# Kernel tuning notes

Hardware: AMD Instinct MI355X
Metric: run time of the kernel (lower is better)

Reference implementation:

```python
import jax, jax.numpy as jnp
import numpy as np

N_CODES, N_EDGES, EMB, N_C, NNZ = 4096, 8192, 128, 4, 65536
ADD_RATIO, TEMP = 0.1, 0.5
MASK_VAL = -1e9


def setup_inputs() -> dict:
    key = jax.random.key(0)
    k1, k2, k3, k4, k5 = jax.random.split(key, 5)
    X = jax.random.normal(k1, (N_CODES, EMB), jnp.float32)
    V = jax.random.randint(k2, (NNZ,), 0, N_CODES)
    E = jax.random.randint(k3, (NNZ,), 0, N_EDGES)
    # incidence matrix has 1s exactly at the (V, E) nonzero entries
    H = jnp.zeros((N_CODES, N_EDGES), jnp.float32).at[V, E].set(1.0)
    p = jnp.clip(jax.random.uniform(k4, (N_CODES, N_EDGES), jnp.float32), 0.05, 0.95)
    cos_weight = jax.random.normal(k5, (N_C, EMB), jnp.float32)
    return {"X": X, "H": H, "V": V, "E": E,
            "incident_mask_prob": p, "cos_weight": cos_weight}


def _l2norm(x):
    # F.normalize(x, p=2, dim=-1, eps=1e-6): x / max(||x||, eps)
    n = jnp.sqrt(jnp.sum(x * x, axis=-1, keepdims=True))
    return x / jnp.maximum(n, 1e-6)


def reference(X, H, V, E, incident_mask_prob, cos_weight):
    num_edges = H.shape[1]
    n_c = cos_weight.shape[0]
    # 1) edge embeddings: scatter-mean of incident code embeddings
    sums = jax.ops.segment_sum(X[V], E, num_segments=num_edges)      # (M, D)
    cnt = jax.ops.segment_sum(jnp.ones((V.shape[0],), X.dtype), E,
                              num_segments=num_edges)                 # (M,)
    eX = sums / jnp.maximum(cnt, 1.0)[:, None]
    # 2) multi-head cosine similarity, mean over heads
    node_m = _l2norm(X[:, None, :] * cos_weight[None])               # (N, h, D)
    edge_m = _l2norm(eX[:, None, :] * cos_weight[None])              # (M, h, D)
    S = jnp.einsum('nhd,mhd->nm', node_m, edge_m) / n_c              # (N, M)
    # mask out existing incidences
    S = S.at[V, E].set(MASK_VAL)
    # 3) global top-k new incidences (k is static)
    k = int(ADD_RATIO * V.shape[0])
    _, idx = jax.lax.top_k(S.reshape(-1), k)
    row = idx // num_edges
    col = idx % num_edges
    delta_H = jnp.zeros_like(H).at[row, col].set(1.0)
    enriched_H = H + delta_H
    # 4) RelaxedBernoulli(temperature, probs).rsample()
    u = jax.random.uniform(jax.random.key(42), H.shape, H.dtype,
                           minval=1e-6, maxval=1.0 - 1e-6)
    logits = (jnp.log(incident_mask_prob) - jnp.log1p(-incident_mask_prob)
              + jnp.log(u) - jnp.log1p(-u)) / TEMP
    incident_mask = jax.nn.sigmoid(logits)
    return enriched_H * incident_mask
```

## Files before the change

### kernel.cpp

```cpp
#include <hip/hip_runtime.h>
#include <math.h>

#define N_CODES 4096
#define N_EDGES 8192
#define EMB     128
#define NHEAD   4
#define NNZ     65536
#define K_TOP   6553
#define S_TOTAL 33554432
#define NBINS   8192
#define CAP2    131072
#define SLACK_BINS 12
#define TIE_CAP 1024

typedef _Float16 f16_t;
typedef __attribute__((ext_vector_type(8))) _Float16 f16x8;
typedef __attribute__((ext_vector_type(4))) float f32x4;

__device__ __forceinline__ unsigned rotl32(unsigned v, int r) {
  return (v << r) | (v >> (32 - r));
}

__device__ float jax_u42(unsigned pos) {
  const unsigned ks0 = 0u, ks1 = 42u, ks2 = 0x1BD11BDAu ^ 0u ^ 42u;
  unsigned x0 = 0u  + ks0;
  unsigned x1 = pos + ks1;
#define TFR(r) { x0 += x1; x1 = rotl32(x1, (r)); x1 ^= x0; }
  TFR(13) TFR(15) TFR(26) TFR(6)   x0 += ks1; x1 += ks2 + 1u;
  TFR(17) TFR(29) TFR(16) TFR(24)  x0 += ks2; x1 += ks0 + 2u;
  TFR(13) TFR(15) TFR(26) TFR(6)   x0 += ks0; x1 += ks1 + 3u;
  TFR(17) TFR(29) TFR(16) TFR(24)  x0 += ks1; x1 += ks2 + 4u;
  TFR(13) TFR(15) TFR(26) TFR(6)   x0 += ks2; x1 += ks0 + 5u;
#undef TFR
  unsigned bits = x0 ^ x1;
  unsigned fb = (bits >> 9) | 0x3f800000u;
  float f = __uint_as_float(fb) - 1.0f;
  const float minv = 1e-6f;
  const float maxv = (float)(1.0 - 1e-6);
  float u = f * (maxv - minv) + minv;
  return fmaxf(minv, u);
}

__device__ float mask_val(float p, unsigned pos) {
  float u = jax_u42(pos);
  float l = (logf(p) - log1pf(-p) + logf(u) - log1pf(-u)) * 2.0f;
  return 1.0f / (1.0f + expf(-l));
}

__device__ __forceinline__ unsigned long long f64key(double v) {
  long long b = __double_as_longlong(v);
  return (b < 0) ? ~(unsigned long long)b
                 : ((unsigned long long)b | 0x8000000000000000ULL);
}

__global__ void count_k(const int* __restrict__ E, int* __restrict__ cnt) {
  int i = blockIdx.x * blockDim.x + threadIdx.x;
  if (i < NNZ) atomicAdd(&cnt[E[i]], 1);
}

__global__ __launch_bounds__(1024) void scan_k(const int* __restrict__ cnt,
                                               int* __restrict__ offs) {
  __shared__ int part[1024];
  int t = threadIdx.x;
  int local[8]; int s = 0;
  for (int j = 0; j < 8; ++j) { local[j] = cnt[t * 8 + j]; s += local[j]; }
  part[t] = s; __syncthreads();
  int v = s;
  for (int o = 1; o < 1024; o <<= 1) {
    int add = (t >= o) ? part[t - o] : 0;
    __syncthreads();
    v += add; part[t] = v;
    __syncthreads();
  }
  int base = v - s;
  for (int j = 0; j < 8; ++j) { offs[t * 8 + j] = base; base += local[j]; }
}

__global__ void scatter_k(const int* __restrict__ E, const int* __restrict__ offs,
                          int* __restrict__ cursor, int* __restrict__ bucket) {
  int i = blockIdx.x * blockDim.x + threadIdx.x;
  if (i < NNZ) {
    int e = E[i];
    int p = atomicAdd(&cursor[e], 1);
    bucket[offs[e] + p] = i;
  }
}

__global__ __launch_bounds__(128) void edge_k(const float* __restrict__ X,
                                              const int* __restrict__ V,
                                              const int* __restrict__ cnt,
                                              const int* __restrict__ offs,
                                              int* __restrict__ bucket,
                                              const float* __restrict__ W,
                                              f16_t* __restrict__ B16) {
  __shared__ int lst[512];
  __shared__ float red[2];
  int m = blockIdx.x, t = threadIdx.x;
  int deg = cnt[m], off = offs[m];
  int n = min(deg, 512);
  for (int j = t; j < n; j += 128) lst[j] = bucket[off + j];
  __syncthreads();
  if (t == 0 && n > 1) {
    for (int a = 1; a < n; ++a) {
      int key = lst[a]; int b = a - 1;
      while (b >= 0 && lst[b] > key) { lst[b + 1] = lst[b]; --b; }
      lst[b + 1] = key;
    }
  }
  __syncthreads();
  for (int j = t; j < n; j += 128) bucket[off + j] = lst[j];
  float s = 0.f;
  for (int j = 0; j < n; ++j) s += X[(size_t)V[lst[j]] * EMB + t];
  float eXd = s / fmaxf((float)deg, 1.0f);
  int lane = t & 63, wv = t >> 6;
  for (int h = 0; h < NHEAD; ++h) {
    float wd = W[h * EMB + t];
    float val = eXd * wd;
    float ss = val * val;
    for (int o = 32; o > 0; o >>= 1) ss += __shfl_down(ss, o, 64);
    if (lane == 0) red[wv] = ss;
    __syncthreads();
    float nh = 1.0f / fmaxf(sqrtf(red[0] + red[1]), 1e-6f);
    B16[(size_t)m * (NHEAD * EMB) + h * EMB + t] = (f16_t)(eXd * wd * wd * nh);
    __syncthreads();
  }
}

__global__ __launch_bounds__(128) void node_k(const float* __restrict__ X,
                                              const float* __restrict__ W,
                                              f16_t* __restrict__ A16) {
  __shared__ float red[2];
  int nid = blockIdx.x, t = threadIdx.x;
  float xd = X[(size_t)nid * EMB + t];
  int lane = t & 63, wv = t >> 6;
  for (int h = 0; h < NHEAD; ++h) {
    float val = xd * W[h * EMB + t];
    float ss = val * val;
    for (int o = 32; o > 0; o >>= 1) ss += __shfl_down(ss, o, 64);
    if (lane == 0) red[wv] = ss;
    __syncthreads();
    float nh = 1.0f / fmaxf(sqrtf(red[0] + red[1]), 1e-6f);
    A16[(size_t)nid * (NHEAD * EMB) + h * EMB + t] = (f16_t)(xd * nh);
    __syncthreads();
  }
}

__global__ __launch_bounds__(256) void gemm_mfma(const f16_t* __restrict__ A16,
                                                 const f16_t* __restrict__ B16,
                                                 float* __restrict__ C) {
  __shared__ __align__(16) f16_t As[128 * 32];
  __shared__ __align__(16) f16_t Bs[128 * 32];
  const int tid  = threadIdx.x;
  const int lane = tid & 63;
  const int wv   = tid >> 6;
  const int m0   = blockIdx.x * 128;
  const int n0   = blockIdx.y * 128;
  const int wr   = (wv >> 1) * 64;
  const int wc   = (wv & 1) * 64;
  const int frow = lane & 15;
  const int fg   = lane >> 4;
  const int sw   = (frow >> 1) & 3;
  const int fo   = ((fg ^ sw) << 3);

  f32x4 acc[4][4];
#pragma unroll
  for (int i = 0; i < 4; ++i)
#pragma unroll
    for (int j = 0; j < 4; ++j) acc[i][j] = (f32x4){0.f, 0.f, 0.f, 0.f};

  for (int k0 = 0; k0 < 512; k0 += 32) {
    __syncthreads();
#pragma unroll
    for (int r = 0; r < 2; ++r) {
      int chunk = r * 256 + wv * 64 + lane;
      int row   = chunk >> 2;
      int cb    = ((chunk & 3) ^ ((chunk >> 3) & 3)) << 3;
      __builtin_amdgcn_global_load_lds(
          (const __attribute__((address_space(1))) void*)
              (A16 + ((size_t)(n0 + row) << 9) + k0 + cb),
          (__attribute__((address_space(3))) void*)
              (As + (size_t)(r * 256 + wv * 64) * 8),
          16, 0, 0);
      __builtin_amdgcn_global_load_lds(
          (const __attribute__((address_space(1))) void*)
              (B16 + ((size_t)(m0 + row) << 9) + k0 + cb),
          (__attribute__((address_space(3))) void*)
              (Bs + (size_t)(r * 256 + wv * 64) * 8),
          16, 0, 0);
    }
    __syncthreads();
    f16x8 a[4], b[4];
#pragma unroll
    for (int i = 0; i < 4; ++i)
      a[i] = *(const f16x8*)(As + (wr + i * 16 + frow) * 32 + fo);
#pragma unroll
    for (int j = 0; j < 4; ++j)
      b[j] = *(const f16x8*)(Bs + (wc + j * 16 + frow) * 32 + fo);
#pragma unroll
    for (int i = 0; i < 4; ++i)
#pragma unroll
      for (int j = 0; j < 4; ++j)
        acc[i][j] = __builtin_amdgcn_mfma_f32_16x16x32_f16(a[i], b[j], acc[i][j], 0, 0, 0);
  }
#pragma unroll
  for (int i = 0; i < 4; ++i)
#pragma unroll
    for (int q = 0; q < 4; ++q) {
      int row = n0 + wr + i * 16 + fg * 4 + q;
      float* Cr = C + (size_t)row * N_EDGES + m0 + wc;
#pragma unroll
      for (int j = 0; j < 4; ++j)
        Cr[j * 16 + frow] = acc[i][j][q] * 0.25f;
    }
}

__global__ void maskset_k(const int* __restrict__ V, const int* __restrict__ E,
                          float* __restrict__ S) {
  int i = blockIdx.x * blockDim.x + threadIdx.x;
  if (i < NNZ) S[(size_t)V[i] * N_EDGES + E[i]] = -1e9f;
}

__global__ __launch_bounds__(256) void hist_k(const float4* __restrict__ S4,
                                              unsigned* __restrict__ ghist) {
  __shared__ unsigned hh[NBINS];
  for (int i = threadIdx.x; i < NBINS; i += 256) hh[i] = 0;
  __syncthreads();
  int stride = gridDim.x * blockDim.x;
  for (int i = blockIdx.x * blockDim.x + threadIdx.x; i < S_TOTAL / 4; i += stride) {
    float4 v = S4[i];
    float vv[4] = {v.x, v.y, v.z, v.w};
#pragma unroll
    for (int c = 0; c < 4; ++c) {
      float bf = fminf(fmaxf((vv[c] + 1.0f) * 4096.0f, 0.0f), (float)(NBINS - 1));
      atomicAdd(&hh[(int)bf], 1u);
    }
  }
  __syncthreads();
  for (int i = threadIdx.x; i < NBINS; i += 256)
    if (hh[i]) atomicAdd(&ghist[i], hh[i]);
}

__global__ __launch_bounds__(1024) void thresh_k(const unsigned* __restrict__ hist,
                                                 float* __restrict__ T_lo) {
  __shared__ unsigned suff[1024];
  int t = threadIdx.x;
  const int G = NBINS / 1024;
  int b0 = t * G;
  unsigned s = 0;
  for (int j = 0; j < G; ++j) s += hist[b0 + j];
  unsigned v = s;
  suff[t] = v; __syncthreads();
  for (int o = 1; o < 1024; o <<= 1) {
    unsigned add = (t + o < 1024) ? suff[t + o] : 0u;
    __syncthreads();
    v += add; suff[t] = v;
    __syncthreads();
  }
  unsigned above = (t < 1023) ? suff[t + 1] : 0u;
  if (above < (unsigned)K_TOP && suff[t] >= (unsigned)K_TOP) {
    unsigned running = above;
    int B = b0;
    for (int b = b0 + G - 1; b >= b0; --b) {
      running += hist[b];
      if (running >= (unsigned)K_TOP) { B = b; break; }
    }
    B = max(B, SLACK_BINS);
    *T_lo = (float)(B - SLACK_BINS) * (1.0f / 4096.0f) - 1.0f;
  }
}

__global__ void collect_k(const float4* __restrict__ S4, const float* __restrict__ T_lo_p,
                          unsigned* __restrict__ counter, int* __restrict__ ci) {
  float T = *T_lo_p;
  int stride = gridDim.x * blockDim.x;
  for (int i = blockIdx.x * blockDim.x + threadIdx.x; i < S_TOTAL / 4; i += stride) {
    float4 v = S4[i];
    float vv[4] = {v.x, v.y, v.z, v.w};
#pragma unroll
    for (int c = 0; c < 4; ++c) {
      if (vv[c] >= T) {
        unsigned j = atomicAdd(counter, 1u);
        if (j < CAP2) ci[j] = i * 4 + c;
      }
    }
  }
}

__global__ __launch_bounds__(256) void rescore_k(const float* __restrict__ X,
                                                 const float* __restrict__ W,
                                                 const int* __restrict__ V,
                                                 const int* __restrict__ cnt,
                                                 const int* __restrict__ offs,
                                                 const int* __restrict__ bucket,
                                                 const int* __restrict__ ci,
                                                 const unsigned* __restrict__ counter,
                                                 unsigned long long* __restrict__ ckey) {
  int C = (int)min(*counter, (unsigned)CAP2);
  int wave = threadIdx.x >> 6, lane = threadIdx.x & 63;
  int j = blockIdx.x * 4 + wave;
  if (j >= C) return;
  int pos = ci[j];
  int n = pos >> 13;
  int m = pos & 8191;
  int deg = cnt[m], off = offs[m];
  int nmem = min(deg, 512);
  double e0 = 0.0, e1 = 0.0;
  for (int q = 0; q < nmem; ++q) {
    const float* xv = X + (size_t)V[bucket[off + q]] * EMB;
    e0 += (double)xv[lane];
    e1 += (double)xv[lane + 64];
  }
  double dd = fmax((double)deg, 1.0);
  e0 /= dd; e1 /= dd;
  const float* xr = X + (size_t)n * EMB;
  double x0 = (double)xr[lane], x1 = (double)xr[lane + 64];
  double s = 0.0;
  for (int h = 0; h < NHEAD; ++h) {
    const float* wr = W + h * EMB;
    double w0 = (double)wr[lane], w1 = (double)wr[lane + 64];
    double xw0 = x0 * w0, xw1 = x1 * w1;
    double ew0 = e0 * w0, ew1 = e1 * w1;
    double an = xw0 * xw0 + xw1 * xw1;
    double ae = ew0 * ew0 + ew1 * ew1;
    double dt = xw0 * ew0 + xw1 * ew1;
    for (int o = 32; o > 0; o >>= 1) {
      an += __shfl_down(an, o, 64);
      ae += __shfl_down(ae, o, 64);
      dt += __shfl_down(dt, o, 64);
    }
    if (lane == 0) {
      double Nn = fmax(sqrt(an), 1e-6);
      double Ne = fmax(sqrt(ae), 1e-6);
      s += dt / (Nn * Ne);
    }
  }
  if (lane == 0) ckey[j] = f64key(s * 0.25);
}

__global__ __launch_bounds__(1024) void kth_k(const unsigned long long* __restrict__ keys,
                                              const unsigned* __restrict__ counter,
                                              unsigned long long* __restrict__ thr) {
  __shared__ unsigned hist[256];
  __shared__ unsigned long long s_prefix;
  __shared__ unsigned s_kleft, s_cgreat;
  int C = (int)min(*counter, (unsigned)CAP2);
  if (threadIdx.x == 0) { s_prefix = 0ULL; s_kleft = K_TOP; s_cgreat = 0u; }
  __syncthreads();
  for (int level = 7; level >= 0; --level) {
    for (int i = threadIdx.x; i < 256; i += 1024) hist[i] = 0;
    __syncthreads();
    unsigned long long prefix = s_prefix;
    unsigned long long pmask = (level == 7) ? 0ULL : (~0ULL << ((level + 1) * 8));
    for (int i = threadIdx.x; i < C; i += 1024) {
      unsigned long long k = keys[i];
      if ((k & pmask) == prefix)
        atomicAdd(&hist[(unsigned)((k >> (level * 8)) & 0xFF)], 1u);
    }
    __syncthreads();
    if (threadIdx.x == 0) {
      unsigned cum = 0; int b = 0;
      for (int i = 255; i >= 0; --i) {
        if (cum + hist[i] >= s_kleft) { b = i; break; }
        cum += hist[i];
      }
      s_prefix |= ((unsigned long long)b << (level * 8));
      s_kleft  -= cum;
      s_cgreat += cum;
    }
    __syncthreads();
  }
  if (threadIdx.x == 0) { thr[0] = s_prefix; thr[1] = (unsigned long long)s_cgreat; }
}

__global__ void write_k(const unsigned long long* __restrict__ keys,
                        const int* __restrict__ ci,
                        const unsigned* __restrict__ counter,
                        const unsigned long long* __restrict__ thr,
                        const float* __restrict__ P, float* __restrict__ out,
                        int* __restrict__ tiebuf, unsigned* __restrict__ tiecnt) {
  int C = (int)min(*counter, (unsigned)CAP2);
  int j = blockIdx.x * blockDim.x + threadIdx.x;
  if (j >= C) return;
  unsigned long long k = keys[j];
  unsigned long long t = thr[0];
  if (k > t) {
    unsigned pos = (unsigned)ci[j];
    out[pos] = mask_val(P[pos], pos);
  } else if (k == t) {
    unsigned q = atomicAdd(tiecnt, 1u);
    if (q < TIE_CAP) tiebuf[q] = ci[j];
  }
}

__global__ __launch_bounds__(256) void tiefin_k(const int* __restrict__ tiebuf,
                                                const unsigned* __restrict__ tiecnt,
                                                const unsigned long long* __restrict__ thr,
                                                const float* __restrict__ P,
                                                float* __restrict__ out) {
  __shared__ int idx[TIE_CAP];
  int T = (int)min(*tiecnt, (unsigned)TIE_CAP);
  int need = K_TOP - (int)thr[1];
  if (need <= 0 || T == 0) return;
  for (int i = threadIdx.x; i < T; i += 256) idx[i] = tiebuf[i];
  __syncthreads();
  if (threadIdx.x == 0 && T > 1) {
    for (int a = 1; a < T; ++a) {
      int key = idx[a]; int b = a - 1;
      while (b >= 0 && idx[b] > key) { idx[b + 1] = idx[b]; --b; }
      idx[b + 1] = key;
    }
  }
  __syncthreads();
  int m = min(need, T);
  for (int i = threadIdx.x; i < m; i += 256) {
    unsigned pos = (unsigned)idx[i];
    out[pos] = mask_val(P[pos], pos);
  }
}

__global__ void scatterH_k(const int* __restrict__ V, const int* __restrict__ E,
                           const float* __restrict__ P, float* __restrict__ out) {
  int i = blockIdx.x * blockDim.x + threadIdx.x;
  if (i >= NNZ) return;
  unsigned pos = (unsigned)V[i] * (unsigned)N_EDGES + (unsigned)E[i];
  out[pos] = mask_val(P[pos], pos);
}

extern "C" void kernel_launch(void* const* d_in, const int* in_sizes, int n_in,
                              void* d_out, int out_size, void* d_ws, size_t ws_size,
                              hipStream_t stream) {
  const float* X = (const float*)d_in[0];
  const int*   V = (const int*)d_in[2];
  const int*   E = (const int*)d_in[3];
  const float* P = (const float*)d_in[4];
  const float* W = (const float*)d_in[5];
  float* S = (float*)d_out;

  char* w = (char*)d_ws;
  int*      cnt      = (int*)(w + 0);
  int*      offs     = (int*)(w + 32768);
  int*      cursor   = (int*)(w + 65536);
  int*      bucket   = (int*)(w + 98304);
  unsigned* hist     = (unsigned*)(w + 360448);
  unsigned* counter  = (unsigned*)(w + 393216);
  float*    T_lo     = (float*)(w + 393220);
  unsigned* tiecnt   = (unsigned*)(w + 393224);
  unsigned long long* thr = (unsigned long long*)(w + 393232);
  int*      cand_idx = (int*)(w + 393472);
  unsigned long long* cand_key = (unsigned long long*)(w + 917760);
  int*      tiebuf   = (int*)(w + 1966336);
  f16_t*    A16      = (f16_t*)(w + 1970432);
  f16_t*    B16      = (f16_t*)(w + 6164736);

  hipMemsetAsync(cnt,     0, 32768, stream);
  hipMemsetAsync(cursor,  0, 32768, stream);
  hipMemsetAsync(hist,    0, NBINS * 4, stream);
  hipMemsetAsync(counter, 0, 48, stream);

  count_k   <<<NNZ / 256, 256, 0, stream>>>(E, cnt);
  scan_k    <<<1, 1024, 0, stream>>>(cnt, offs);
  scatter_k <<<NNZ / 256, 256, 0, stream>>>(E, offs, cursor, bucket);
  edge_k    <<<N_EDGES, 128, 0, stream>>>(X, V, cnt, offs, bucket, W, B16);
  node_k    <<<N_CODES, 128, 0, stream>>>(X, W, A16);
  gemm_mfma <<<dim3(N_EDGES / 128, N_CODES / 128), 256, 0, stream>>>(A16, B16, S);
  maskset_k <<<NNZ / 256, 256, 0, stream>>>(V, E, S);
  hist_k    <<<512, 256, 0, stream>>>((const float4*)S, hist);
  thresh_k  <<<1, 1024, 0, stream>>>(hist, T_lo);
  collect_k <<<1024, 256, 0, stream>>>((const float4*)S, T_lo, counter, cand_idx);
  rescore_k <<<CAP2 / 4, 256, 0, stream>>>(X, W, V, cnt, offs, bucket,
                                           cand_idx, counter, cand_key);
  kth_k     <<<1, 1024, 0, stream>>>(cand_key, counter, thr);
  hipMemsetAsync(d_out, 0, (size_t)S_TOTAL * 4, stream);
  write_k   <<<CAP2 / 256, 256, 0, stream>>>(cand_key, cand_idx, counter, thr,
                                             P, S, tiebuf, tiecnt);
  tiefin_k  <<<1, 256, 0, stream>>>(tiebuf, tiecnt, thr, P, S);
  scatterH_k<<<NNZ / 256, 256, 0, stream>>>(V, E, P, S);
}
```

Before: 583.5 us.

## Fuse histogram and candidate collection into recomputed GEMM, dropping the S matrix

The full 4096x8192 similarity matrix is no longer written to memory and read back twice. The GEMM now runs twice: the first pass builds the score histogram in LDS and flushes it into 16 replicated global histograms, and the second pass uses the threshold to collect candidates straight from registers. A separate kernel recomputes the scores of existing incidences and subtracts them from the histogram, and the collect pass skips existing incidences by scanning each edge's bucket. This trades roughly 128 MB of writes plus two full reads for a second GEMM, per-element LDS atomics and a membership scan per candidate.

```diff
diff --git a/kernel.cpp b/kernel.cpp
--- a/kernel.cpp
+++ b/kernel.cpp
@@ -9,6 +9,7 @@
 #define K_TOP   6553
 #define S_TOTAL 33554432
 #define NBINS   8192
+#define NREP    16
 #define CAP2    131072
 #define SLACK_BINS 12
 #define TIE_CAP 1024
@@ -145,11 +146,12 @@
   }
 }
 
-__global__ __launch_bounds__(256) void gemm_mfma(const f16_t* __restrict__ A16,
+__global__ __launch_bounds__(256) void gemm_hist(const f16_t* __restrict__ A16,
                                                  const f16_t* __restrict__ B16,
-                                                 float* __restrict__ C) {
+                                                 unsigned* __restrict__ ghist) {
   __shared__ __align__(16) f16_t As[128 * 32];
   __shared__ __align__(16) f16_t Bs[128 * 32];
+  __shared__ unsigned hh[NBINS];
   const int tid  = threadIdx.x;
   const int lane = tid & 63;
   const int wv   = tid >> 6;
@@ -161,6 +163,8 @@
   const int fg   = lane >> 4;
   const int sw   = (frow >> 1) & 3;
   const int fo   = ((fg ^ sw) << 3);
+
+  for (int i = tid; i < NBINS; i += 256) hh[i] = 0;
 
   f32x4 acc[4][4];
 #pragma unroll
@@ -205,85 +209,162 @@
 #pragma unroll
   for (int i = 0; i < 4; ++i)
 #pragma unroll
-    for (int q = 0; q < 4; ++q) {
-      int row = n0 + wr + i * 16 + fg * 4 + q;
-      float* Cr = C + (size_t)row * N_EDGES + m0 + wc;
-#pragma unroll
-      for (int j = 0; j < 4; ++j)
-        Cr[j * 16 + frow] = acc[i][j][q] * 0.25f;
-    }
-}
-
-__global__ void maskset_k(const int* __restrict__ V, const int* __restrict__ E,
-                          float* __restrict__ S) {
-  int i = blockIdx.x * blockDim.x + threadIdx.x;
-  if (i < NNZ) S[(size_t)V[i] * N_EDGES + E[i]] = -1e9f;
-}
-
-__global__ __launch_bounds__(256) void hist_k(const float4* __restrict__ S4,
+    for (int j = 0; j < 4; ++j)
+#pragma unroll
+      for (int q = 0; q < 4; ++q) {
+        float v = acc[i][j][q] * 0.25f;
+        float bf = fminf(fmaxf((v + 1.0f) * 4096.0f, 0.0f), (float)(NBINS - 1));
+        atomicAdd(&hh[(int)bf], 1u);
+      }
+  __syncthreads();
+  unsigned* gh = ghist + (size_t)(blockIdx.x & (NREP - 1)) * NBINS;
+  for (int i = tid; i < NBINS; i += 256) {
+    unsigned c = hh[i];
+    if (c) atomicAdd(&gh[i], c);
+  }
+}
+
+__global__ __launch_bounds__(256) void corr_k(const f16_t* __restrict__ A16,
+                                              const f16_t* __restrict__ B16,
+                                              const int* __restrict__ V,
+                                              const int* __restrict__ E,
                                               unsigned* __restrict__ ghist) {
-  __shared__ unsigned hh[NBINS];
-  for (int i = threadIdx.x; i < NBINS; i += 256) hh[i] = 0;
-  __syncthreads();
-  int stride = gridDim.x * blockDim.x;
-  for (int i = blockIdx.x * blockDim.x + threadIdx.x; i < S_TOTAL / 4; i += stride) {
-    float4 v = S4[i];
-    float vv[4] = {v.x, v.y, v.z, v.w};
-#pragma unroll
-    for (int c = 0; c < 4; ++c) {
-      float bf = fminf(fmaxf((vv[c] + 1.0f) * 4096.0f, 0.0f), (float)(NBINS - 1));
-      atomicAdd(&hh[(int)bf], 1u);
-    }
-  }
-  __syncthreads();
-  for (int i = threadIdx.x; i < NBINS; i += 256)
-    if (hh[i]) atomicAdd(&ghist[i], hh[i]);
+  int wave = threadIdx.x >> 6, lane = threadIdx.x & 63;
+  int j = blockIdx.x * 4 + wave;
+  if (j >= NNZ) return;
+  int n = V[j], m = E[j];
+  f16x8 a = *(const f16x8*)(A16 + ((size_t)n << 9) + lane * 8);
+  f16x8 b = *(const f16x8*)(B16 + ((size_t)m << 9) + lane * 8);
+  float s = 0.f;
+#pragma unroll
+  for (int c = 0; c < 8; ++c) s += (float)a[c] * (float)b[c];
+  for (int o = 32; o > 0; o >>= 1) s += __shfl_down(s, o, 64);
+  if (lane == 0) {
+    float v = s * 0.25f;
+    float bf = fminf(fmaxf((v + 1.0f) * 4096.0f, 0.0f), (float)(NBINS - 1));
+    atomicAdd(&ghist[(size_t)(j & (NREP - 1)) * NBINS + (int)bf], (unsigned)-1);
+  }
 }
 
 __global__ __launch_bounds__(1024) void thresh_k(const unsigned* __restrict__ hist,
                                                  float* __restrict__ T_lo) {
-  __shared__ unsigned suff[1024];
+  __shared__ int suff[1024];
   int t = threadIdx.x;
   const int G = NBINS / 1024;
   int b0 = t * G;
-  unsigned s = 0;
-  for (int j = 0; j < G; ++j) s += hist[b0 + j];
-  unsigned v = s;
+  int s = 0;
+  for (int j = 0; j < G; ++j) {
+    unsigned tb = 0;
+    for (int r = 0; r < NREP; ++r) tb += hist[(size_t)r * NBINS + b0 + j];
+    s += (int)tb;
+  }
+  int v = s;
   suff[t] = v; __syncthreads();
   for (int o = 1; o < 1024; o <<= 1) {
-    unsigned add = (t + o < 1024) ? suff[t + o] : 0u;
+    int add = (t + o < 1024) ? suff[t + o] : 0;
     __syncthreads();
     v += add; suff[t] = v;
     __syncthreads();
   }
-  unsigned above = (t < 1023) ? suff[t + 1] : 0u;
-  if (above < (unsigned)K_TOP && suff[t] >= (unsigned)K_TOP) {
-    unsigned running = above;
+  int above = (t < 1023) ? suff[t + 1] : 0;
+  if (above < K_TOP && suff[t] >= K_TOP) {
+    int running = above;
     int B = b0;
     for (int b = b0 + G - 1; b >= b0; --b) {
-      running += hist[b];
-      if (running >= (unsigned)K_TOP) { B = b; break; }
+      unsigned tb = 0;
+      for (int r = 0; r < NREP; ++r) tb += hist[(size_t)r * NBINS + b];
+      running += (int)tb;
+      if (running >= K_TOP) { B = b; break; }
     }
     B = max(B, SLACK_BINS);
     *T_lo = (float)(B - SLACK_BINS) * (1.0f / 4096.0f) - 1.0f;
   }
 }
 
-__global__ void collect_k(const float4* __restrict__ S4, const float* __restrict__ T_lo_p,
-                          unsigned* __restrict__ counter, int* __restrict__ ci) {
-  float T = *T_lo_p;
-  int stride = gridDim.x * blockDim.x;
-  for (int i = blockIdx.x * blockDim.x + threadIdx.x; i < S_TOTAL / 4; i += stride) {
-    float4 v = S4[i];
-    float vv[4] = {v.x, v.y, v.z, v.w};
-#pragma unroll
-    for (int c = 0; c < 4; ++c) {
-      if (vv[c] >= T) {
-        unsigned j = atomicAdd(counter, 1u);
-        if (j < CAP2) ci[j] = i * 4 + c;
+__global__ __launch_bounds__(256) void gemm_collect(const f16_t* __restrict__ A16,
+                                                    const f16_t* __restrict__ B16,
+                                                    const float* __restrict__ T_lo_p,
+                                                    const int* __restrict__ V,
+                                                    const int* __restrict__ cnt,
+                                                    const int* __restrict__ offs,
+                                                    const int* __restrict__ bucket,
+                                                    unsigned* __restrict__ counter,
+                                                    int* __restrict__ ci) {
+  __shared__ __align__(16) f16_t As[128 * 32];
+  __shared__ __align__(16) f16_t Bs[128 * 32];
+  const int tid  = threadIdx.x;
+  const int lane = tid & 63;
+  const int wv   = tid >> 6;
+  const int m0   = blockIdx.x * 128;
+  const int n0   = blockIdx.y * 128;
+  const int wr   = (wv >> 1) * 64;
+  const int wc   = (wv & 1) * 64;
+  const int frow = lane & 15;
+  const int fg   = lane >> 4;
+  const int sw   = (frow >> 1) & 3;
+  const int fo   = ((fg ^ sw) << 3);
+  const float T  = *T_lo_p;
+
+  f32x4 acc[4][4];
+#pragma unroll
+  for (int i = 0; i < 4; ++i)
+#pragma unroll
+    for (int j = 0; j < 4; ++j) acc[i][j] = (f32x4){0.f, 0.f, 0.f, 0.f};
+
+  for (int k0 = 0; k0 < 512; k0 += 32) {
+    __syncthreads();
+#pragma unroll
+    for (int r = 0; r < 2; ++r) {
+      int chunk = r * 256 + wv * 64 + lane;
+      int row   = chunk >> 2;
+      int cb    = ((chunk & 3) ^ ((chunk >> 3) & 3)) << 3;
+      __builtin_amdgcn_global_load_lds(
+          (const __attribute__((address_space(1))) void*)
+              (A16 + ((size_t)(n0 + row) << 9) + k0 + cb),
+          (__attribute__((address_space(3))) void*)
+              (As + (size_t)(r * 256 + wv * 64) * 8),
+          16, 0, 0);
+      __builtin_amdgcn_global_load_lds(
+          (const __attribute__((address_space(1))) void*)
+              (B16 + ((size_t)(m0 + row) << 9) + k0 + cb),
+          (__attribute__((address_space(3))) void*)
+              (Bs + (size_t)(r * 256 + wv * 64) * 8),
+          16, 0, 0);
+    }
+    __syncthreads();
+    f16x8 a[4], b[4];
+#pragma unroll
+    for (int i = 0; i < 4; ++i)
+      a[i] = *(const f16x8*)(As + (wr + i * 16 + frow) * 32 + fo);
+#pragma unroll
+    for (int j = 0; j < 4; ++j)
+      b[j] = *(const f16x8*)(Bs + (wc + j * 16 + frow) * 32 + fo);
+#pragma unroll
+    for (int i = 0; i < 4; ++i)
+#pragma unroll
+      for (int j = 0; j < 4; ++j)
+        acc[i][j] = __builtin_amdgcn_mfma_f32_16x16x32_f16(a[i], b[j], acc[i][j], 0, 0, 0);
+  }
+#pragma unroll
+  for (int i = 0; i < 4; ++i)
+#pragma unroll
+    for (int j = 0; j < 4; ++j)
+#pragma unroll
+      for (int q = 0; q < 4; ++q) {
+        float v = acc[i][j][q] * 0.25f;
+        if (v >= T) {
+          int m   = m0 + wc + j * 16 + frow;
+          int row = n0 + wr + i * 16 + fg * 4 + q;
+          int deg = min(cnt[m], 512), off = offs[m];
+          bool member = false;
+          for (int u = 0; u < deg; ++u)
+            if (V[bucket[off + u]] == row) { member = true; break; }
+          if (!member) {
+            unsigned p = atomicAdd(counter, 1u);
+            if (p < CAP2) ci[p] = (row << 13) | m;
+          }
+        }
       }
-    }
-  }
 }
 
 __global__ __launch_bounds__(256) void rescore_k(const float* __restrict__ X,
@@ -434,45 +515,45 @@
   const int*   E = (const int*)d_in[3];
   const float* P = (const float*)d_in[4];
   const float* W = (const float*)d_in[5];
-  float* S = (float*)d_out;
+  float* OUT = (float*)d_out;
 
   char* w = (char*)d_ws;
   int*      cnt      = (int*)(w + 0);
   int*      offs     = (int*)(w + 32768);
   int*      cursor   = (int*)(w + 65536);
   int*      bucket   = (int*)(w + 98304);
-  unsigned* hist     = (unsigned*)(w + 360448);
-  unsigned* counter  = (unsigned*)(w + 393216);
-  float*    T_lo     = (float*)(w + 393220);
-  unsigned* tiecnt   = (unsigned*)(w + 393224);
-  unsigned long long* thr = (unsigned long long*)(w + 393232);
-  int*      cand_idx = (int*)(w + 393472);
-  unsigned long long* cand_key = (unsigned long long*)(w + 917760);
-  int*      tiebuf   = (int*)(w + 1966336);
-  f16_t*    A16      = (f16_t*)(w + 1970432);
-  f16_t*    B16      = (f16_t*)(w + 6164736);
+  unsigned* counter  = (unsigned*)(w + 360448);
+  float*    T_lo     = (float*)(w + 360452);
+  unsigned* tiecnt   = (unsigned*)(w + 360456);
+  unsigned long long* thr = (unsigned long long*)(w + 360464);
+  int*      cand_idx = (int*)(w + 360704);
+  unsigned* ghist    = (unsigned*)(w + 360704);
+  unsigned long long* cand_key = (unsigned long long*)(w + 884992);
+  int*      tiebuf   = (int*)(w + 1933568);
+  f16_t*    A16      = (f16_t*)(w + 1937664);
+  f16_t*    B16      = (f16_t*)(w + 6131968);
 
   hipMemsetAsync(cnt,     0, 32768, stream);
   hipMemsetAsync(cursor,  0, 32768, stream);
-  hipMemsetAsync(hist,    0, NBINS * 4, stream);
-  hipMemsetAsync(counter, 0, 48, stream);
-
-  count_k   <<<NNZ / 256, 256, 0, stream>>>(E, cnt);
-  scan_k    <<<1, 1024, 0, stream>>>(cnt, offs);
-  scatter_k <<<NNZ / 256, 256, 0, stream>>>(E, offs, cursor, bucket);
-  edge_k    <<<N_EDGES, 128, 0, stream>>>(X, V, cnt, offs, bucket, W, B16);
-  node_k    <<<N_CODES, 128, 0, stream>>>(X, W, A16);
-  gemm_mfma <<<dim3(N_EDGES / 128, N_CODES / 128), 256, 0, stream>>>(A16, B16, S);
-  maskset_k <<<NNZ / 256, 256, 0, stream>>>(V, E, S);
-  hist_k    <<<512, 256, 0, stream>>>((const float4*)S, hist);
-  thresh_k  <<<1, 1024, 0, stream>>>(hist, T_lo);
-  collect_k <<<1024, 256, 0, stream>>>((const float4*)S, T_lo, counter, cand_idx);
-  rescore_k <<<CAP2 / 4, 256, 0, stream>>>(X, W, V, cnt, offs, bucket,
-                                           cand_idx, counter, cand_key);
-  kth_k     <<<1, 1024, 0, stream>>>(cand_key, counter, thr);
-  hipMemsetAsync(d_out, 0, (size_t)S_TOTAL * 4, stream);
-  write_k   <<<CAP2 / 256, 256, 0, stream>>>(cand_key, cand_idx, counter, thr,
-                                             P, S, tiebuf, tiecnt);
-  tiefin_k  <<<1, 256, 0, stream>>>(tiebuf, tiecnt, thr, P, S);
-  scatterH_k<<<NNZ / 256, 256, 0, stream>>>(V, E, P, S);
-}
+  hipMemsetAsync((void*)(w + 360448), 0, 64, stream);
+  hipMemsetAsync(ghist,   0, (size_t)NREP * NBINS * 4, stream);
+  hipMemsetAsync(d_out,   0, (size_t)S_TOTAL * 4, stream);
+
+  count_k    <<<NNZ / 256, 256, 0, stream>>>(E, cnt);
+  scan_k     <<<1, 1024, 0, stream>>>(cnt, offs);
+  scatter_k  <<<NNZ / 256, 256, 0, stream>>>(E, offs, cursor, bucket);
+  edge_k     <<<N_EDGES, 128, 0, stream>>>(X, V, cnt, offs, bucket, W, B16);
+  node_k     <<<N_CODES, 128, 0, stream>>>(X, W, A16);
+  gemm_hist  <<<dim3(N_EDGES / 128, N_CODES / 128), 256, 0, stream>>>(A16, B16, ghist);
+  corr_k     <<<NNZ / 4, 256, 0, stream>>>(A16, B16, V, E, ghist);
+  thresh_k   <<<1, 1024, 0, stream>>>(ghist, T_lo);
+  gemm_collect<<<dim3(N_EDGES / 128, N_CODES / 128), 256, 0, stream>>>(
+      A16, B16, T_lo, V, cnt, offs, bucket, counter, cand_idx);
+  rescore_k  <<<CAP2 / 4, 256, 0, stream>>>(X, W, V, cnt, offs, bucket,
+                                            cand_idx, counter, cand_key);
+  kth_k      <<<1, 1024, 0, stream>>>(cand_key, counter, thr);
+  write_k    <<<CAP2 / 256, 256, 0, stream>>>(cand_key, cand_idx, counter, thr,
+                                              P, OUT, tiebuf, tiecnt);
+  tiefin_k   <<<1, 256, 0, stream>>>(tiebuf, tiecnt, thr, P, OUT);
+  scatterH_k <<<NNZ / 256, 256, 0, stream>>>(V, E, P, OUT);
+}
```

Result: slower. 620.4 us (+6.3%).
